# Performance work log

Measured on AMD Instinct MI355X. Metric: run time of the kernel, lower is better.

The kernel has to match this reference:

```python
import jax, jax.numpy as jnp
import numpy as np

TWO_PI = 2.0 * np.pi


def setup_inputs() -> dict:
    key = jax.random.key(0)
    ks = jax.random.split(key, 6)
    n1 = n2 = n3 = 20
    nk, ni, nspin = 4, 16, 2
    # Invertible, physically plausible lattice (~8 Bohr cubic cell + jitter)
    A = jnp.eye(3, dtype=jnp.float32) * 8.0 + 0.05 * jax.random.normal(ks[0], (3, 3), jnp.float32)
    k_grid = 0.1 * jax.random.normal(ks[1], (nk, 3), jnp.float32)
    cg_real = jax.random.normal(ks[2], (nspin, nk, ni, n1, n2, n3), jnp.float32)
    cg_imag = jax.random.normal(ks[3], (nspin, nk, ni, n1, n2, n3), jnp.float32)
    # Real-space evaluation grid: fractional coords in [0,1)^3 mapped through A
    frac = jax.random.uniform(ks[4], (n1, n2, n3, 3), jnp.float32)
    r = frac @ A
    return {"A": A, "k_grid": k_grid, "cg_real": cg_real, "cg_imag": cg_imag, "r": r}


def reference(A, k_grid, cg_real, cg_imag, r):
    # cg: [spin, nk, ni, n1, n2, n3] complex plane-wave coefficients
    cg = cg_real + 1j * cg_imag
    n1, n2, n3 = cg.shape[-3:]
    # Integer FFT frequency mesh m -> reciprocal-lattice vectors G = m @ B,
    # B rows are reciprocal basis: B = 2*pi * inv(A)^T  (A rows = lattice vecs)
    f1 = jnp.fft.fftfreq(n1) * n1
    f2 = jnp.fft.fftfreq(n2) * n2
    f3 = jnp.fft.fftfreq(n3) * n3
    m = jnp.stack(jnp.meshgrid(f1, f2, f3, indexing="ij"), axis=-1).astype(A.dtype)  # [n1,n2,n3,3]
    B = TWO_PI * jnp.linalg.inv(A).T
    G = (m @ B).reshape(-1, 3)                      # [nG, 3]
    vol = jnp.abs(jnp.linalg.det(A))
    Rf = r.reshape(-1, 3)                           # [nR, 3]
    # Plane-wave synthesis: psi_{s,k,i}(r) = exp(i k.r)/sqrt(vol) * sum_G c_G exp(i G.r)
    # (equivalent to the triple-nested vmap over the grid dims, fully vectorized)
    phase_g = jnp.exp(1j * (Rf @ G.T))              # [nR, nG] complex
    dens = cg.reshape(*cg.shape[:3], -1)            # [spin, nk, ni, nG]
    psi = jnp.einsum("skin,rn->skir", dens, phase_g)  # [spin, nk, ni, nR]
    phase_k = jnp.exp(1j * (Rf @ k_grid.T))         # [nR, nk]
    psi = psi * jnp.moveaxis(phase_k, 0, -1)[None, :, None, :]
    psi = psi / jnp.sqrt(vol).astype(psi.real.dtype)
    # [spin, nk, ni, n1, n2, n3] -- matches moveaxis(range(3), range(-3,0))
    return psi.reshape(*cg.shape[:3], *r.shape[:-1])
```

## Files before the change

kernel.cpp:

```cpp
#include <hip/hip_runtime.h>

typedef __attribute__((ext_vector_type(4))) float f32x4;
typedef __attribute__((ext_vector_type(8))) short s16x8;

#define NG     8000
#define NRPT   8000
#define NSKIN  128
#define NT     64
#define KCH    800
#define NKC    10
#define NTILES 25
#define NROUND 10
#define NSLOT  6
#define TPB    256
#define WS_TILE_B 16384
#define WS_NEED   ((size_t)NKC*NTILES*WS_TILE_B)

__device__ __forceinline__ float sin_rev(float u){ float r; asm("v_sin_f32 %0, %1" : "=v"(r) : "v"(u)); return r; }
__device__ __forceinline__ float cos_rev(float u){ float r; asm("v_cos_f32 %0, %1" : "=v"(r) : "v"(u)); return r; }
__device__ __forceinline__ unsigned int cvt_pk(float lo, float hi){
    unsigned int r; asm("v_cvt_pk_bf16_f32 %0, %1, %2" : "=v"(r) : "v"(lo), "v"(hi)); return r;
}
__device__ __forceinline__ s16x8 bneg(s16x8 v){
    int4 u = *(int4*)&v;
    u.x ^= 0x80008000; u.y ^= 0x80008000; u.z ^= 0x80008000; u.w ^= 0x80008000;
    return *(s16x8*)&u;
}
__device__ __forceinline__ s16x8 pack8(float4 v0, float4 v1){
    union { s16x8 v; uint4 u; } r;
    r.u.x = cvt_pk(v0.x,v0.y); r.u.y = cvt_pk(v0.z,v0.w);
    r.u.z = cvt_pk(v1.x,v1.y); r.u.w = cvt_pk(v1.z,v1.w);
    return r.v;
}
__device__ __forceinline__ int swz(int row, int kg){
    return row*64 + ((kg ^ ((row>>1)&3))<<4);
}

__global__ __launch_bounds__(256) void bloch_prepass(
    const float* __restrict__ cgr, const float* __restrict__ cgi,
    char* __restrict__ ws)
{
    int gid = blockIdx.x*256 + threadIdx.x;
    if (gid >= NKC*NTILES*2*8*64) return;
    int lane  = gid & 63;
    int rb8   = (gid >> 6) & 7;
    int plane = (gid >> 9) & 1;
    int tile  = gid >> 10;
    int row   = rb8*16 + (lane & 15);
    int k     = tile*32 + (lane >> 4)*8;
    const float* src = plane ? cgi : cgr;
    const float4 v0 = *(const float4*)&src[(size_t)row*NG + k];
    const float4 v1 = *(const float4*)&src[(size_t)row*NG + k + 4];
    uint4 p;
    p.x = cvt_pk(v0.x, v0.y); p.y = cvt_pk(v0.z, v0.w);
    p.z = cvt_pk(v1.x, v1.y); p.w = cvt_pk(v1.z, v1.w);
    *(uint4*)(ws + (size_t)gid*16) = p;
}

template<bool PRE>
__global__ __launch_bounds__(TPB, 2) void bloch12(
    const float* __restrict__ Amat, const float* __restrict__ kgrid,
    const float* __restrict__ cgr,  const float* __restrict__ cgi,
    const float* __restrict__ rpts, const char* __restrict__ ws,
    float* __restrict__ out, int out_size)
{
    __shared__ __align__(16) char smem[NSLOT*8192];
    __shared__ float fracS[NT][4];
    __shared__ float invAS[9];
    __shared__ float scaleS;

    const int tid = threadIdx.x;
    const int bid = blockIdx.x;
    const int kc  = bid >> 7;
    const int rb  = bid & 127;
    if (rb >= 125) return;
    const int r_base = rb * NT;

    if (tid == 0) {
        float a00=Amat[0],a01=Amat[1],a02=Amat[2];
        float a10=Amat[3],a11=Amat[4],a12=Amat[5];
        float a20=Amat[6],a21=Amat[7],a22=Amat[8];
        float c00 =  (a11*a22 - a12*a21);
        float c01 = -(a10*a22 - a12*a20);
        float c02 =  (a10*a21 - a11*a20);
        float det = a00*c00 + a01*c01 + a02*c02;
        float id  = 1.0f/det;
        invAS[0] =  c00*id;
        invAS[1] = -(a01*a22 - a02*a21)*id;
        invAS[2] =  (a01*a12 - a02*a11)*id;
        invAS[3] =  c01*id;
        invAS[4] =  (a00*a22 - a02*a20)*id;
        invAS[5] = -(a00*a12 - a02*a10)*id;
        invAS[6] =  c02*id;
        invAS[7] = -(a00*a21 - a01*a20)*id;
        invAS[8] =  (a00*a11 - a01*a10)*id;
        scaleS   = rsqrtf(fabsf(det));
    }
    __syncthreads();

    if (tid < NT) {
        int rg = r_base + tid;
        float r0 = rpts[rg*3+0], r1 = rpts[rg*3+1], r2 = rpts[rg*3+2];
        fracS[tid][0] = r0*invAS[0] + r1*invAS[3] + r2*invAS[6];
        fracS[tid][1] = r0*invAS[1] + r1*invAS[4] + r2*invAS[7];
        fracS[tid][2] = r0*invAS[2] + r1*invAS[5] + r2*invAS[8];
    }
    __syncthreads();

    f32x4 accRe[4][2], accIm[4][2];
    #pragma unroll
    for (int mi = 0; mi < 4; ++mi)
        #pragma unroll
        for (int ni = 0; ni < 2; ++ni) {
            accRe[mi][ni] = (f32x4){0.f,0.f,0.f,0.f};
            accIm[mi][ni] = (f32x4){0.f,0.f,0.f,0.f};
        }

    const int lane = tid & 63;
    const int wid  = tid >> 6;
    const int wm   = wid >> 1;
    const int wn   = wid & 1;
    const int frow = lane & 15;
    const int kq   = lane >> 4;
    const int bOff = swz(wn*32 + frow, kq);

    const float f0r = fracS[lane][0], f1r = fracS[lane][1], f2r = fracS[lane][2];
    float u1 = f2r - floorf(f2r);
    const float w1c = cos_rev(u1), w1s = sin_rev(u1);
    float yd = -20.0f * f2r; yd -= floorf(yd);
    const float wdc = cos_rev(yd), wds = sin_rev(yd);
    const float w1wdc = w1c*wdc - w1s*wds;
    const float w1wds = w1c*wds + w1s*wdc;

    auto stageRing = [&](int R){
        int i12 = kc*40 + 4*R + wid;
        int i1  = (i12 * 3277) >> 16;
        int i2  = i12 - i1*20;
        float m1 = (float)(i1 - (i1 >= 10 ? 20 : 0));
        float m2 = (float)(i2 - (i2 >= 10 ? 20 : 0));
        float y0 = m1*f0r + m2*f1r; y0 -= floorf(y0);
        float cc = cos_rev(y0), cs = sin_rev(y0);
        unsigned int pkc[10], pks[10];
        #pragma unroll
        for (int jj = 0; jj < 10; ++jj) {
            float ac = cc, as_ = cs;
            { float nc = cc*w1c - cs*w1s, ns = cc*w1s + cs*w1c; cc=nc; cs=ns; }
            pkc[jj] = cvt_pk(ac, cc);
            pks[jj] = cvt_pk(as_, cs);
            if (jj < 9) {
                if (jj == 4) { float nc = cc*w1wdc - cs*w1wds, ns = cc*w1wds + cs*w1wdc; cc=nc; cs=ns; }
                else         { float nc = cc*w1c  - cs*w1s,  ns = cc*w1s  + cs*w1c;  cc=nc; cs=ns; }
            }
        }
        int gg = (80*R + wid*20) % 192;
        int gA = gg >> 3;
        auto adr = [&](int g, int p)->char* {
            if (g >= 24) g -= 24;
            return smem + (g>>2)*8192 + p*4096 + swz(lane, g&3);
        };
        if ((gg & 7) == 0) {
            *(uint4*)adr(gA,0)   = make_uint4(pkc[0],pkc[1],pkc[2],pkc[3]);
            *(uint4*)adr(gA+1,0) = make_uint4(pkc[4],pkc[5],pkc[6],pkc[7]);
            *(uint2*)adr(gA+2,0) = make_uint2(pkc[8],pkc[9]);
            *(uint4*)adr(gA,1)   = make_uint4(pks[0],pks[1],pks[2],pks[3]);
            *(uint4*)adr(gA+1,1) = make_uint4(pks[4],pks[5],pks[6],pks[7]);
            *(uint2*)adr(gA+2,1) = make_uint2(pks[8],pks[9]);
        } else {
            *(uint2*)(adr(gA,0)+8) = make_uint2(pkc[0],pkc[1]);
            *(uint4*)adr(gA+1,0)   = make_uint4(pkc[2],pkc[3],pkc[4],pkc[5]);
            *(uint4*)adr(gA+2,0)   = make_uint4(pkc[6],pkc[7],pkc[8],pkc[9]);
            *(uint2*)(adr(gA,1)+8) = make_uint2(pks[0],pks[1]);
            *(uint4*)adr(gA+1,1)   = make_uint4(pks[2],pks[3],pks[4],pks[5]);
            *(uint4*)adr(gA+2,1)   = make_uint4(pks[6],pks[7],pks[8],pks[9]);
        }
    };

    s16x8 arfP[4], aifP[4];
    auto loadA = [&](int t){
        if (PRE) {
            const char* tb = ws + (size_t)(kc*NTILES + t)*WS_TILE_B + lane*16;
            #pragma unroll
            for (int mi = 0; mi < 4; ++mi) {
                arfP[mi] = *(const s16x8*)(tb +        (wm*4 + mi)*1024);
                aifP[mi] = *(const s16x8*)(tb + 8192 + (wm*4 + mi)*1024);
            }
        } else {
            #pragma unroll
            for (int mi = 0; mi < 4; ++mi) {
                int row = wm*64 + mi*16 + frow;
                int k   = kc*KCH + t*32 + kq*8;
                const float* pr_ = &cgr[(size_t)row*NG + k];
                const float* pi_ = &cgi[(size_t)row*NG + k];
                arfP[mi] = pack8(*(const float4*)pr_, *(const float4*)(pr_+4));
                aifP[mi] = pack8(*(const float4*)pi_, *(const float4*)(pi_+4));
            }
        }
    };

    loadA(0);
    stageRing(0);
    __syncthreads();

    int tcur = 0, slot = 0;
    #pragma unroll 1
    for (int R = 0; R < NROUND; ++R) {
        if (R + 1 < NROUND) stageRing(R + 1);
        const int t_hi = (5*R + 5) >> 1;
        #pragma unroll 1
        while (tcur < t_hi) {
            const char* base = smem + slot*8192;
            s16x8 bcf[2], bsf[2], bsnf[2];
            #pragma unroll
            for (int ni = 0; ni < 2; ++ni) {
                bcf[ni]  = *(const s16x8*)(base +        bOff + ni*1024);
                bsf[ni]  = *(const s16x8*)(base + 4096 + bOff + ni*1024);
                bsnf[ni] = bneg(bsf[ni]);
            }
            __builtin_amdgcn_s_setprio(1);
            #pragma unroll
            for (int mi = 0; mi < 4; ++mi)
                #pragma unroll
                for (int ni = 0; ni < 2; ++ni) {
                    accRe[mi][ni] = __builtin_amdgcn_mfma_f32_16x16x32_bf16(arfP[mi], bcf[ni],  accRe[mi][ni], 0, 0, 0);
                    accRe[mi][ni] = __builtin_amdgcn_mfma_f32_16x16x32_bf16(aifP[mi], bsnf[ni], accRe[mi][ni], 0, 0, 0);
                    accIm[mi][ni] = __builtin_amdgcn_mfma_f32_16x16x32_bf16(arfP[mi], bsf[ni],  accIm[mi][ni], 0, 0, 0);
                    accIm[mi][ni] = __builtin_amdgcn_mfma_f32_16x16x32_bf16(aifP[mi], bcf[ni],  accIm[mi][ni], 0, 0, 0);
                }
            __builtin_amdgcn_s_setprio(0);
            ++tcur;
            if (tcur < NTILES) loadA(tcur);
            ++slot; if (slot == NSLOT) slot = 0;
        }
        __syncthreads();
    }

    float2* ekr = (float2*)smem;
    {
        int col = tid >> 2, kidx = tid & 3;
        int rg = r_base + col;
        float r0 = rpts[rg*3+0], r1 = rpts[rg*3+1], r2 = rpts[rg*3+2];
        float ang = (r0*kgrid[kidx*3+0] + r1*kgrid[kidx*3+1] + r2*kgrid[kidx*3+2])
                    * 0.15915494309189535f;
        float u = ang - floorf(ang);
        ekr[col*4+kidx] = make_float2(cos_rev(u), sin_rev(u));
    }
    __syncthreads();

    const bool write_imag = (out_size >= 2*NSKIN*NRPT);
    const float scale = scaleS;
    #pragma unroll
    for (int mi = 0; mi < 4; ++mi) {
        const int m0 = wm*64 + mi*16;
        const int kidx = (m0 >> 4) & 3;
        #pragma unroll
        for (int ni = 0; ni < 2; ++ni) {
            int col = wn*32 + ni*16 + frow;
            int rg = r_base + col;
            float2 e = ekr[col*4+kidx];
            float ck = e.x, sk = e.y;
            #pragma unroll
            for (int v = 0; v < 4; ++v) {
                int sg = m0 + kq*4 + v;
                float re = accRe[mi][ni][v];
                float im = accIm[mi][ni][v];
                float orr = (re*ck - im*sk) * scale;
                size_t lin = (size_t)sg * NRPT + rg;
                if (write_imag) {
                    float oi = (re*sk + im*ck) * scale;
                    size_t idx = lin * 2;
                    if (idx + 1 < (size_t)out_size) {
                        atomicAdd(&out[idx],   orr);
                        atomicAdd(&out[idx+1], oi);
                    }
                } else {
                    atomicAdd(&out[lin], orr);
                }
            }
        }
    }
}

extern "C" void kernel_launch(void* const* d_in, const int* in_sizes, int n_in,
                              void* d_out, int out_size, void* d_ws, size_t ws_size,
                              hipStream_t stream) {
    const float* Amat  = (const float*)d_in[0];
    const float* kgrid = (const float*)d_in[1];
    const float* cgr   = (const float*)d_in[2];
    const float* cgi   = (const float*)d_in[3];
    const float* rpts  = (const float*)d_in[4];
    float* out = (float*)d_out;

    hipMemsetAsync(d_out, 0, (size_t)out_size * sizeof(float), stream);

    const bool use_pre = (ws_size >= WS_NEED);
    dim3 grid(NKC * 128);
    if (use_pre) {
        bloch_prepass<<<dim3(NKC*NTILES*2*8*64/256), 256, 0, stream>>>(cgr, cgi, (char*)d_ws);
        bloch12<true><<<grid, TPB, 0, stream>>>(Amat, kgrid, cgr, cgi, rpts,
                                                (const char*)d_ws, out, out_size);
    } else {
        bloch12<false><<<grid, TPB, 0, stream>>>(Amat, kgrid, cgr, cgi, rpts,
                                                 nullptr, out, out_size);
    }
}
```

Measured before the change: 89.97 us.

## Generate phase-factor B fragments in registers instead of a shared-memory ring

Removes the 48KB shared-memory staging ring and its per-round barriers. Each wave now computes its own cos/sin phase fragments directly in MFMA operand layout, using angle-recurrence rotations that handle the wrap of the third index. Freeing the LDS lets launch bounds go from 2 to 3 blocks per SM. The cost is extra transcendental and rotation arithmetic per tile, since each wave recomputes B values that were previously shared across waves. There is also more register pressure under the tighter launch bound.

```diff
diff --git a/kernel.cpp b/kernel.cpp
--- a/kernel.cpp
+++ b/kernel.cpp
@@ -10,8 +10,6 @@
 #define KCH    800
 #define NKC    10
 #define NTILES 25
-#define NROUND 10
-#define NSLOT  6
 #define TPB    256
 #define WS_TILE_B 16384
 #define WS_NEED   ((size_t)NKC*NTILES*WS_TILE_B)
@@ -21,19 +19,13 @@
 __device__ __forceinline__ unsigned int cvt_pk(float lo, float hi){
     unsigned int r; asm("v_cvt_pk_bf16_f32 %0, %1, %2" : "=v"(r) : "v"(lo), "v"(hi)); return r;
 }
-__device__ __forceinline__ s16x8 bneg(s16x8 v){
-    int4 u = *(int4*)&v;
-    u.x ^= 0x80008000; u.y ^= 0x80008000; u.z ^= 0x80008000; u.w ^= 0x80008000;
-    return *(s16x8*)&u;
+__device__ __forceinline__ s16x8 pack_u4(unsigned int a, unsigned int b, unsigned int c, unsigned int d){
+    union { s16x8 v; uint4 u; } r;
+    r.u = make_uint4(a,b,c,d);
+    return r.v;
 }
 __device__ __forceinline__ s16x8 pack8(float4 v0, float4 v1){
-    union { s16x8 v; uint4 u; } r;
-    r.u.x = cvt_pk(v0.x,v0.y); r.u.y = cvt_pk(v0.z,v0.w);
-    r.u.z = cvt_pk(v1.x,v1.y); r.u.w = cvt_pk(v1.z,v1.w);
-    return r.v;
-}
-__device__ __forceinline__ int swz(int row, int kg){
-    return row*64 + ((kg ^ ((row>>1)&3))<<4);
+    return pack_u4(cvt_pk(v0.x,v0.y), cvt_pk(v0.z,v0.w), cvt_pk(v1.x,v1.y), cvt_pk(v1.z,v1.w));
 }
 
 __global__ __launch_bounds__(256) void bloch_prepass(
@@ -58,14 +50,14 @@
 }
 
 template<bool PRE>
-__global__ __launch_bounds__(TPB, 2) void bloch12(
+__global__ __launch_bounds__(TPB, 3) void bloch15(
     const float* __restrict__ Amat, const float* __restrict__ kgrid,
     const float* __restrict__ cgr,  const float* __restrict__ cgi,
     const float* __restrict__ rpts, const char* __restrict__ ws,
     float* __restrict__ out, int out_size)
 {
-    __shared__ __align__(16) char smem[NSLOT*8192];
     __shared__ float fracS[NT][4];
+    __shared__ float2 ekrS[NT][4];
     __shared__ float invAS[9];
     __shared__ float scaleS;
 
@@ -122,58 +114,19 @@
     const int wn   = wid & 1;
     const int frow = lane & 15;
     const int kq   = lane >> 4;
-    const int bOff = swz(wn*32 + frow, kq);
-
-    const float f0r = fracS[lane][0], f1r = fracS[lane][1], f2r = fracS[lane][2];
-    float u1 = f2r - floorf(f2r);
-    const float w1c = cos_rev(u1), w1s = sin_rev(u1);
-    float yd = -20.0f * f2r; yd -= floorf(yd);
-    const float wdc = cos_rev(yd), wds = sin_rev(yd);
-    const float w1wdc = w1c*wdc - w1s*wds;
-    const float w1wds = w1c*wds + w1s*wdc;
-
-    auto stageRing = [&](int R){
-        int i12 = kc*40 + 4*R + wid;
-        int i1  = (i12 * 3277) >> 16;
-        int i2  = i12 - i1*20;
-        float m1 = (float)(i1 - (i1 >= 10 ? 20 : 0));
-        float m2 = (float)(i2 - (i2 >= 10 ? 20 : 0));
-        float y0 = m1*f0r + m2*f1r; y0 -= floorf(y0);
-        float cc = cos_rev(y0), cs = sin_rev(y0);
-        unsigned int pkc[10], pks[10];
-        #pragma unroll
-        for (int jj = 0; jj < 10; ++jj) {
-            float ac = cc, as_ = cs;
-            { float nc = cc*w1c - cs*w1s, ns = cc*w1s + cs*w1c; cc=nc; cs=ns; }
-            pkc[jj] = cvt_pk(ac, cc);
-            pks[jj] = cvt_pk(as_, cs);
-            if (jj < 9) {
-                if (jj == 4) { float nc = cc*w1wdc - cs*w1wds, ns = cc*w1wds + cs*w1wdc; cc=nc; cs=ns; }
-                else         { float nc = cc*w1c  - cs*w1s,  ns = cc*w1s  + cs*w1c;  cc=nc; cs=ns; }
-            }
-        }
-        int gg = (80*R + wid*20) % 192;
-        int gA = gg >> 3;
-        auto adr = [&](int g, int p)->char* {
-            if (g >= 24) g -= 24;
-            return smem + (g>>2)*8192 + p*4096 + swz(lane, g&3);
-        };
-        if ((gg & 7) == 0) {
-            *(uint4*)adr(gA,0)   = make_uint4(pkc[0],pkc[1],pkc[2],pkc[3]);
-            *(uint4*)adr(gA+1,0) = make_uint4(pkc[4],pkc[5],pkc[6],pkc[7]);
-            *(uint2*)adr(gA+2,0) = make_uint2(pkc[8],pkc[9]);
-            *(uint4*)adr(gA,1)   = make_uint4(pks[0],pks[1],pks[2],pks[3]);
-            *(uint4*)adr(gA+1,1) = make_uint4(pks[4],pks[5],pks[6],pks[7]);
-            *(uint2*)adr(gA+2,1) = make_uint2(pks[8],pks[9]);
-        } else {
-            *(uint2*)(adr(gA,0)+8) = make_uint2(pkc[0],pkc[1]);
-            *(uint4*)adr(gA+1,0)   = make_uint4(pkc[2],pkc[3],pkc[4],pkc[5]);
-            *(uint4*)adr(gA+2,0)   = make_uint4(pkc[6],pkc[7],pkc[8],pkc[9]);
-            *(uint2*)(adr(gA,1)+8) = make_uint2(pks[0],pks[1]);
-            *(uint4*)adr(gA+1,1)   = make_uint4(pks[2],pks[3],pks[4],pks[5]);
-            *(uint4*)adr(gA+2,1)   = make_uint4(pks[6],pks[7],pks[8],pks[9]);
-        }
-    };
+
+    float f0c[2], f1c[2], f2c[2], w1cc[2], w1sc[2], wdcc[2], wdsc[2];
+    #pragma unroll
+    for (int ni = 0; ni < 2; ++ni) {
+        int col = wn*32 + ni*16 + frow;
+        f0c[ni] = fracS[col][0]; f1c[ni] = fracS[col][1]; f2c[ni] = fracS[col][2];
+        float u1 = f2c[ni] - floorf(f2c[ni]);
+        w1cc[ni] = cos_rev(u1); w1sc[ni] = sin_rev(u1);
+        float yd = -20.0f * f2c[ni]; yd -= floorf(yd);
+        float wc_ = cos_rev(yd), ws_ = sin_rev(yd);
+        wdcc[ni] = w1cc[ni]*wc_ - w1sc[ni]*ws_;
+        wdsc[ni] = w1cc[ni]*ws_ + w1sc[ni]*wc_;
+    }
 
     s16x8 arfP[4], aifP[4];
     auto loadA = [&](int t){
@@ -198,43 +151,65 @@
     };
 
     loadA(0);
-    stageRing(0);
-    __syncthreads();
-
-    int tcur = 0, slot = 0;
+
     #pragma unroll 1
-    for (int R = 0; R < NROUND; ++R) {
-        if (R + 1 < NROUND) stageRing(R + 1);
-        const int t_hi = (5*R + 5) >> 1;
-        #pragma unroll 1
-        while (tcur < t_hi) {
-            const char* base = smem + slot*8192;
-            s16x8 bcf[2], bsf[2], bsnf[2];
+    for (int t = 0; t < NTILES; ++t) {
+        s16x8 bcf[2], bsf[2], bsnf[2];
+        const int g0 = kc*KCH + t*32 + kq*8;
+        const int i12  = (g0 * 3277) >> 16;
+        const int i3_0 = g0 - i12*20;
+        const int i1a  = (i12 * 3277) >> 16; const int i2a = i12 - i1a*20;
+        const int i12b = i12 + 1;
+        const int i1b  = (i12b * 3277) >> 16; const int i2b = i12b - i1b*20;
+        const float m1a = (float)(i1a - (i1a >= 10 ? 20 : 0));
+        const float m2a = (float)(i2a - (i2a >= 10 ? 20 : 0));
+        const float dm1 = (float)((i1b - (i1b >= 10 ? 20 : 0))) - m1a;
+        const float dm2 = (float)((i2b - (i2b >= 10 ? 20 : 0))) - m2a;
+        const float m30 = (float)(i3_0 - (i3_0 >= 10 ? 20 : 0));
+        #pragma unroll
+        for (int ni = 0; ni < 2; ++ni) {
+            float y0 = m1a*f0c[ni] + m2a*f1c[ni] + m30*f2c[ni]; y0 -= floorf(y0);
+            float cc = cos_rev(y0), cs = sin_rev(y0);
+            float rd = dm1*f0c[ni] + dm2*f1c[ni]; rd -= floorf(rd);
+            float rc = cos_rev(rd), rs = sin_rev(rd);
+            float wXc = w1cc[ni]*rc - w1sc[ni]*rs;
+            float wXs = w1cc[ni]*rs + w1sc[ni]*rc;
+            float bcv[8], bsv[8];
+            bcv[0] = cc; bsv[0] = cs;
+            #pragma unroll
+            for (int j = 1; j < 8; ++j) {
+                bool cB = (i3_0 == 20 - j);
+                bool cD = (i3_0 == 10 - j);
+                float mc = cB ? wXc : (cD ? wdcc[ni] : w1cc[ni]);
+                float ms = cB ? wXs : (cD ? wdsc[ni] : w1sc[ni]);
+                float nc = cc*mc - cs*ms;
+                float ns = cc*ms + cs*mc;
+                cc = nc; cs = ns;
+                bcv[j] = cc; bsv[j] = cs;
+            }
+            bcf[ni] = pack_u4(cvt_pk(bcv[0],bcv[1]), cvt_pk(bcv[2],bcv[3]),
+                              cvt_pk(bcv[4],bcv[5]), cvt_pk(bcv[6],bcv[7]));
+            bsf[ni] = pack_u4(cvt_pk(bsv[0],bsv[1]), cvt_pk(bsv[2],bsv[3]),
+                              cvt_pk(bsv[4],bsv[5]), cvt_pk(bsv[6],bsv[7]));
+            bsnf[ni] = pack_u4(cvt_pk(-bsv[0],-bsv[1]), cvt_pk(-bsv[2],-bsv[3]),
+                               cvt_pk(-bsv[4],-bsv[5]), cvt_pk(-bsv[6],-bsv[7]));
+        }
+
+        __builtin_amdgcn_s_setprio(1);
+        #pragma unroll
+        for (int mi = 0; mi < 4; ++mi)
             #pragma unroll
             for (int ni = 0; ni < 2; ++ni) {
-                bcf[ni]  = *(const s16x8*)(base +        bOff + ni*1024);
-                bsf[ni]  = *(const s16x8*)(base + 4096 + bOff + ni*1024);
-                bsnf[ni] = bneg(bsf[ni]);
-            }
-            __builtin_amdgcn_s_setprio(1);
-            #pragma unroll
-            for (int mi = 0; mi < 4; ++mi)
-                #pragma unroll
-                for (int ni = 0; ni < 2; ++ni) {
-                    accRe[mi][ni] = __builtin_amdgcn_mfma_f32_16x16x32_bf16(arfP[mi], bcf[ni],  accRe[mi][ni], 0, 0, 0);
-                    accRe[mi][ni] = __builtin_amdgcn_mfma_f32_16x16x32_bf16(aifP[mi], bsnf[ni], accRe[mi][ni], 0, 0, 0);
-                    accIm[mi][ni] = __builtin_amdgcn_mfma_f32_16x16x32_bf16(arfP[mi], bsf[ni],  accIm[mi][ni], 0, 0, 0);
-                    accIm[mi][ni] = __builtin_amdgcn_mfma_f32_16x16x32_bf16(aifP[mi], bcf[ni],  accIm[mi][ni], 0, 0, 0);
-                }
-            __builtin_amdgcn_s_setprio(0);
-            ++tcur;
-            if (tcur < NTILES) loadA(tcur);
-            ++slot; if (slot == NSLOT) slot = 0;
-        }
-        __syncthreads();
-    }
-
-    float2* ekr = (float2*)smem;
+                accRe[mi][ni] = __builtin_amdgcn_mfma_f32_16x16x32_bf16(arfP[mi], bcf[ni],  accRe[mi][ni], 0, 0, 0);
+                accRe[mi][ni] = __builtin_amdgcn_mfma_f32_16x16x32_bf16(aifP[mi], bsnf[ni], accRe[mi][ni], 0, 0, 0);
+                accIm[mi][ni] = __builtin_amdgcn_mfma_f32_16x16x32_bf16(arfP[mi], bsf[ni],  accIm[mi][ni], 0, 0, 0);
+                accIm[mi][ni] = __builtin_amdgcn_mfma_f32_16x16x32_bf16(aifP[mi], bcf[ni],  accIm[mi][ni], 0, 0, 0);
+            }
+        __builtin_amdgcn_s_setprio(0);
+
+        if (t + 1 < NTILES) loadA(t + 1);
+    }
+
     {
         int col = tid >> 2, kidx = tid & 3;
         int rg = r_base + col;
@@ -242,7 +217,7 @@
         float ang = (r0*kgrid[kidx*3+0] + r1*kgrid[kidx*3+1] + r2*kgrid[kidx*3+2])
                     * 0.15915494309189535f;
         float u = ang - floorf(ang);
-        ekr[col*4+kidx] = make_float2(cos_rev(u), sin_rev(u));
+        ekrS[col][kidx] = make_float2(cos_rev(u), sin_rev(u));
     }
     __syncthreads();
 
@@ -256,7 +231,7 @@
         for (int ni = 0; ni < 2; ++ni) {
             int col = wn*32 + ni*16 + frow;
             int rg = r_base + col;
-            float2 e = ekr[col*4+kidx];
+            float2 e = ekrS[col][kidx];
             float ck = e.x, sk = e.y;
             #pragma unroll
             for (int v = 0; v < 4; ++v) {
@@ -267,10 +242,10 @@
                 size_t lin = (size_t)sg * NRPT + rg;
                 if (write_imag) {
                     float oi = (re*sk + im*ck) * scale;
-                    size_t idx = lin * 2;
-                    if (idx + 1 < (size_t)out_size) {
-                        atomicAdd(&out[idx],   orr);
-                        atomicAdd(&out[idx+1], oi);
+                    size_t idx2 = lin * 2;
+                    if (idx2 + 1 < (size_t)out_size) {
+                        atomicAdd(&out[idx2],   orr);
+                        atomicAdd(&out[idx2+1], oi);
                     }
                 } else {
                     atomicAdd(&out[lin], orr);
@@ -296,10 +271,10 @@
     dim3 grid(NKC * 128);
     if (use_pre) {
         bloch_prepass<<<dim3(NKC*NTILES*2*8*64/256), 256, 0, stream>>>(cgr, cgi, (char*)d_ws);
-        bloch12<true><<<grid, TPB, 0, stream>>>(Amat, kgrid, cgr, cgi, rpts,
+        bloch15<true><<<grid, TPB, 0, stream>>>(Amat, kgrid, cgr, cgi, rpts,
                                                 (const char*)d_ws, out, out_size);
     } else {
-        bloch12<false><<<grid, TPB, 0, stream>>>(Amat, kgrid, cgr, cgi, rpts,
+        bloch15<false><<<grid, TPB, 0, stream>>>(Amat, kgrid, cgr, cgi, rpts,
                                                  nullptr, out, out_size);
     }
 }
```

New measurement: 113.5 us. 26.1% more time.
